# Kernel tuning notes

Hardware: AMD Instinct MI355X
Metric: run time of the kernel (lower is better)

## Reference

```python
import jax, jax.numpy as jnp
import numpy as np

# ---- Cl(3,0) geometric-algebra Cayley table (8 blades: 1,e1,e2,e3,e12,e13,e23,e123) ----
# T[k, i, j] = sign s.t. blade_i * blade_j = sign * blade_k (exactly 8 (i,j) pairs per k).

def _build_cayley():
    masks = [0b000, 0b001, 0b010, 0b100, 0b011, 0b101, 0b110, 0b111]
    T = np.zeros((8, 8, 8), np.float32)
    for i, a in enumerate(masks):
        for j, b in enumerate(masks):
            k = masks.index(a ^ b)
            aa, s = a >> 1, 0
            while aa:
                s += bin(aa & b).count('1')
                aa >>= 1
            T[k, i, j] = -1.0 if (s & 1) else 1.0
    return jnp.asarray(T)

CAYLEY = _build_cayley()
LN_EPS = 1e-5  # torch LayerNorm default


def _layer_norm(x, w, b):
    mu = jnp.mean(x, axis=-1, keepdims=True)
    var = jnp.var(x, axis=-1, keepdims=True)
    return (x - mu) * jax.lax.rsqrt(var + LN_EPS) * w + b


def _expert_forward(x_e, p_in, p_out, iw, gg, w_gate, w_up, w_down, lnw, lnb, out_w, out_b):
    # x_e: (C, D); p_in: (D, ED); per-round params indexed [r]
    C = x_e.shape[0]
    DB = lnw.shape[-1]
    mv = (x_e @ p_in).reshape(C, 8, DB)  # (C, n_blades, d_blade)
    n_rounds = iw.shape[0]
    for r in range(n_rounds):
        w = jax.nn.sigmoid(iw[r]).reshape(8, 8)          # interaction weights w[i,j]
        gate = jax.nn.sigmoid(gg[r])                      # scalar geo gate
        # geo[n,k,d] = sum_{i,j} sign[k,i,j] * w[i,j] * mv[n,i,d] * mv[n,j,d]
        geo = jnp.einsum('kij,ij,nid,njd->nkd', CAYLEY, w, mv, mv)
        mixed = gate * geo + (1.0 - gate) * mv
        flat = _layer_norm(mixed, lnw[r], lnb[r])         # LN over d_blade
        h = jax.nn.silu(flat @ w_gate[r]) * (flat @ w_up[r])  # SwiGLU
        mv = mv + h @ w_down[r]                           # residual
    out = mv.reshape(C, -1) @ p_out                       # (C, D)
    return _layer_norm(out, out_w, out_b)


def setup_inputs() -> dict:
    key = jax.random.key(0)
    ks = jax.random.split(key, 8)
    E, D, NB, DB, R, F = 16, 1024, 8, 64, 2, 256
    ED = NB * DB
    N = 32768
    C = N // E
    std = 0.02
    return {
        'x_sorted': jax.random.normal(ks[0], (N, D), jnp.float32),
        'proj_in': jax.random.normal(ks[1], (E, D, ED), jnp.float32) * std,
        'proj_out': jax.random.normal(ks[2], (E, ED, D), jnp.float32) * std,
        'interaction_weights': jnp.ones((E, R, 64), jnp.float32) * 0.1,
        'geo_gates': jnp.ones((E, R), jnp.float32) * 0.5,
        'ffn_gate': jax.random.normal(ks[3], (E, R, DB, F), jnp.float32) * std,
        'ffn_up': jax.random.normal(ks[4], (E, R, DB, F), jnp.float32) * std,
        'ffn_down': jax.random.normal(ks[5], (E, R, F, DB), jnp.float32) * std,
        'ffn_ln_w': jnp.ones((E, R, DB), jnp.float32),
        'ffn_ln_b': jnp.zeros((E, R, DB), jnp.float32),
        'out_ln_w': jnp.ones((D,), jnp.float32),
        'out_ln_b': jnp.zeros((D,), jnp.float32),
        'expert_offsets': jnp.arange(E, dtype=jnp.int32) * C,
        'expert_counts': jnp.full((E,), C, dtype=jnp.int32),
    }


def reference(x_sorted, proj_in, proj_out, interaction_weights, geo_gates,
              ffn_gate, ffn_up, ffn_down, ffn_ln_w, ffn_ln_b,
              out_ln_w, out_ln_b, expert_offsets, expert_counts):
    E = proj_in.shape[0]
    N, D = x_sorted.shape
    C = N // E  # balanced routing: equal tokens per expert (static shapes)
    idx = expert_offsets[:, None].astype(jnp.int32) + jnp.arange(C, dtype=jnp.int32)[None, :]
    x_b = x_sorted[idx]  # (E, C, D) gather of sorted tokens per expert
    y_b = jax.vmap(_expert_forward,
                   in_axes=(0, 0, 0, 0, 0, 0, 0, 0, 0, 0, None, None))(
        x_b, proj_in, proj_out, interaction_weights, geo_gates,
        ffn_gate, ffn_up, ffn_down, ffn_ln_w, ffn_ln_b, out_ln_w, out_ln_b)
    y = jnp.zeros_like(x_sorted).at[idx.reshape(-1)].set(y_b.reshape(-1, D))
    return y
```

## Files before the change

kernel.cpp:

```cpp
#include <hip/hip_runtime.h>

#define DEV __device__ __forceinline__

typedef __attribute__((ext_vector_type(4))) float f32x4;
typedef __attribute__((ext_vector_type(2))) float f32x2;
typedef __attribute__((ext_vector_type(8))) short bf16x8;


DEV unsigned short f2bf(float f) {
  union { float f; unsigned u; } v; v.f = f;
  unsigned r = v.u + 0x7fffu + ((v.u >> 16) & 1u);
  return (unsigned short)(r >> 16);
}

DEV unsigned pk2bf(float lo, float hi) {
  unsigned r;
  asm("v_cvt_pk_bf16_f32 %0, %1, %2" : "=v"(r) : "v"(lo), "v"(hi));
  return r;
}
DEV unsigned short f2bf1(float v) { return (unsigned short)pk2bf(v, v); }

DEV float bf2f(unsigned short b) {
  union { unsigned u; float f; } v; v.u = ((unsigned)b) << 16; return v.f;
}

DEV float frcp(float x) { return __builtin_amdgcn_rcpf(x); }

DEV void sbar() { asm volatile("s_barrier" ::: "memory"); }
DEV void wait_lgkm0() { asm volatile("s_waitcnt lgkmcnt(0)" ::: "memory"); }
DEV void wait_vm0() { asm volatile("s_waitcnt vmcnt(0)" ::: "memory"); }

DEV void async16(const unsigned short* g, unsigned short* l) {
  __builtin_amdgcn_global_load_lds(
      (__attribute__((address_space(1))) const unsigned int*)g,
      (__attribute__((address_space(3))) unsigned int*)l, 16, 0, 0);
}

DEV long tiled_off(long n, int k, int K) {
  return (n >> 3) * (8L * K) + (long)(((k >> 3) * 64) + ((int)(n & 7)) * 8 + (k & 7));
}

DEV bf16x8 ld_frag(const char* s, int row, int hi) {
  return *(const bf16x8*)(s + ((row >> 3) * 512 + hi * 128 + (row & 7) * 16));
}

__host__ __device__ constexpr int km_(int i) { return i==0?0:i==1?1:i==2?2:i==3?4:i==4?3:i==5?5:i==6?6:7; }
__host__ __device__ constexpr int pc_(int x) { int c = 0; while (x) { c += x & 1; x >>= 1; } return c; }
__host__ __device__ constexpr int KIDX(int i, int j) { return km_(km_(i) ^ km_(j)); }
__host__ __device__ constexpr int CSGN(int i, int j) {
  int a = km_(i), b = km_(j), aa = a >> 1, s = 0;
  while (aa) { s += pc_(aa & b); aa >>= 1; }
  return (s & 1) ? -1 : 1;
}
__host__ __device__ constexpr int PIDX(int i, int j) {
  return 8 * i - (i * (i - 1)) / 2 + (j - i);
}

__global__ __launch_bounds__(64) void geoprep_k(const float* __restrict__ iw,
                                                const float* __restrict__ gg,
                                                float* __restrict__ wcomb) {
  int er = threadIdx.x;
  if (er >= 32) return;
  const float* w = iw + er * 64;
  float gate = frcp(1.f + __expf(-gg[er]));
  float* c = wcomb + er * 40;
  int p = 0;
  for (int i = 0; i < 8; ++i)
    for (int j = i; j < 8; ++j) {
      float v = (float)CSGN(i, j) * frcp(1.f + __expf(-w[i * 8 + j]));
      if (j > i) v += (float)CSGN(j, i) * frcp(1.f + __expf(-w[j * 8 + i]));
      c[p++] = gate * v;
    }
  c[36] = 1.f - gate;
}

template<int TI>
__global__ __launch_bounds__(256) void transpose_k(const float* __restrict__ in,
                                                   unsigned short* __restrict__ out,
                                                   int Rr, int Cc) {
  __shared__ unsigned short tile[32][33];
  const float* ib = in + (long)blockIdx.z * Rr * Cc;
  unsigned short* ob = out + (long)blockIdx.z * Rr * Cc;
  int r0 = blockIdx.y * 32, c0 = blockIdx.x * 32;
  int tr = threadIdx.x >> 5, tc = threadIdx.x & 31;
#pragma unroll
  for (int i = 0; i < 4; ++i) {
    int r = tr + i * 8;
    tile[r][tc] = f2bf(ib[(long)(r0 + r) * Cc + c0 + tc]);
  }
  __syncthreads();
#pragma unroll
  for (int i = 0; i < 4; ++i) {
    int c = tr + i * 8;
    int row = c0 + c;
    int k = r0 + tc;
    if (TI == 0) ob[(long)row * Rr + k] = tile[tc][c];
    else ob[(long)row * Rr + (k ^ ((row & 7) << 3))] = tile[tc][c];
  }
}

__global__ __launch_bounds__(256) void trans_big_k(const float* __restrict__ in,
                                                   unsigned short* __restrict__ out,
                                                   int Rr, int Cc) {
  __shared__ float t[64][64];
  const float* ib = in + (long)blockIdx.z * Rr * Cc;
  unsigned short* ob = out + (long)blockIdx.z * (long)Rr * Cc;
  int k0 = blockIdx.y * 64, n0 = blockIdx.x * 64;
  int tid = threadIdx.x;
#pragma unroll
  for (int p = 0; p < 4; ++p) {
    int idx = p * 256 + tid;
    int kr = idx >> 4, nc = (idx & 15) * 4;
    *(float4*)&t[kr][nc] = *(const float4*)(ib + (long)(k0 + kr) * Cc + n0 + nc);
  }
  __syncthreads();
#pragma unroll
  for (int p = 0; p < 2; ++p) {
    int idx = p * 256 + tid;
    int n = idx & 63, kc = idx >> 6;
    float v[8];
#pragma unroll
    for (int u = 0; u < 8; ++u) v[u] = t[kc * 8 + u][n];
    uint4 o;
    o.x = pk2bf(v[0], v[1]); o.y = pk2bf(v[2], v[3]);
    o.z = pk2bf(v[4], v[5]); o.w = pk2bf(v[6], v[7]);
    *(uint4*)(ob + tiled_off(n0 + n, k0 + kc * 8, Rr)) = o;
  }
}

__global__ __launch_bounds__(512, 1) void gemm_in_k(const float* __restrict__ X,
                                                    const unsigned short* __restrict__ Bw,
                                                    unsigned short* __restrict__ MvB,
                                                    const int* __restrict__ offs) {
  extern __shared__ char smem[];
  int bid = blockIdx.x;
  int wg = (bid & 7) * 32 + (bid >> 3);
  int e = wg >> 4, rem = wg & 15, bm = rem >> 1, bn = rem & 1;
  int tid = threadIdx.x, wid = tid >> 6, lane = tid & 63;
  int wm = (wid >> 2) * 128, wn = (wid & 3) * 64;
  int ri = lane & 15, hi = lane >> 4;
  long rowbase = (long)offs[e] + bm * 256;
  long bw = (long)e * 64 + bn * 32;

  auto STGB = [&](int p) {
    int t = p >> 1, s = p & 1, b = t & 1;
    char* dst = smem + b * 65536 + 32768 + s * 16384;
#pragma unroll
    for (int i = 0; i < 2; ++i) {
      int d = i * 512 + tid;
      async16(Bw + (bw + (d >> 5)) * 8192 +
                  (long)((t * 8 + s * 4 + ((d >> 3) & 3)) * 64 + (d & 7) * 8),
              (unsigned short*)(dst + d * 16));
    }
  };
  auto A_LOAD = [&](int p, float4 ar[2][2]) {
    int t = p >> 1, s = p & 1;
#pragma unroll
    for (int i = 0; i < 2; ++i) {
      int d = i * 512 + tid;
      const float* src = X + (rowbase + ((d >> 5) * 8 + (d & 7))) * 1024 +
                         t * 64 + s * 32 + ((d >> 3) & 3) * 8;
      ar[i][0] = *(const float4*)src;
      ar[i][1] = *(const float4*)(src + 4);
    }
  };
  auto A_WRITE = [&](int p, float4 ar[2][2]) {
    int t = p >> 1, s = p & 1, b = t & 1;
    char* dst = smem + b * 65536 + s * 16384;
#pragma unroll
    for (int i = 0; i < 2; ++i) {
      int d = i * 512 + tid;
      uint4 o;
      o.x = pk2bf(ar[i][0].x, ar[i][0].y);
      o.y = pk2bf(ar[i][0].z, ar[i][0].w);
      o.z = pk2bf(ar[i][1].x, ar[i][1].y);
      o.w = pk2bf(ar[i][1].z, ar[i][1].w);
      *(uint4*)(dst + d * 16) = o;
    }
  };

  f32x4 acc[8][4];
#pragma unroll
  for (int i = 0; i < 8; ++i)
#pragma unroll
    for (int j = 0; j < 4; ++j) acc[i][j] = (f32x4){0.f, 0.f, 0.f, 0.f};

  float4 ar[2][2];
  A_LOAD(0, ar); STGB(0); STGB(1);
  A_WRITE(0, ar);
  A_LOAD(1, ar);
  A_WRITE(1, ar);
  wait_lgkm0();

#pragma unroll 2
  for (int p = 0; p < 32; ++p) {
    int t = p >> 1, s = p & 1, c = t & 1;
    if (p < 30) { A_LOAD(p + 2, ar); STGB(p + 2); }
    if (p < 30) asm volatile("s_waitcnt vmcnt(8)" ::: "memory");
    else if (p == 30) asm volatile("s_waitcnt vmcnt(2)" ::: "memory");
    else asm volatile("s_waitcnt vmcnt(0)" ::: "memory");
    sbar();
    const char* cA = smem + c * 65536 + s * 16384;
    const char* cB = smem + c * 65536 + 32768 + s * 16384;
    bf16x8 a[8], b[4];
#pragma unroll
    for (int i = 0; i < 8; ++i) a[i] = ld_frag(cA, wm + i * 16 + ri, hi);
#pragma unroll
    for (int j = 0; j < 4; ++j) b[j] = ld_frag(cB, wn + j * 16 + ri, hi);
    __builtin_amdgcn_s_setprio(1);
#pragma unroll
    for (int i = 0; i < 8; ++i)
#pragma unroll
      for (int j = 0; j < 4; ++j)
        acc[i][j] = __builtin_amdgcn_mfma_f32_16x16x32_bf16(a[i], b[j], acc[i][j], 0, 0, 0);
    __builtin_amdgcn_s_setprio(0);
    if (p < 30) A_WRITE(p + 2, ar);
    wait_lgkm0();
  }

  unsigned short* Cb = MvB + ((long)e * 2048 + (long)bm * 256) * 512 + bn * 256;
#pragma unroll
  for (int i = 0; i < 8; ++i)
#pragma unroll
    for (int j = 0; j < 4; ++j)
#pragma unroll
      for (int rr = 0; rr < 4; ++rr)
        Cb[(long)(wm + i * 16 + hi * 4 + rr) * 512 + wn + j * 16 + ri] =
            f2bf1(acc[i][j][rr]);
}

__global__ __launch_bounds__(256, 3) void rounds_k(
    const unsigned short* __restrict__ MvB, const unsigned short* __restrict__ WgT,
    const unsigned short* __restrict__ WuT, const unsigned short* __restrict__ WdT,
    const float* __restrict__ wcomb, const float* __restrict__ lnw,
    const float* __restrict__ lnb, unsigned short* __restrict__ Mvb) {
  extern __shared__ char smem[];
  int tid = threadIdx.x, wid = tid >> 6, lane = tid & 63;
  char* sFH = smem + wid * 4096;
  char* sMv = smem + 16384 + wid * 4096;
  char* sW  = smem + 32768;

  int bid = blockIdx.x;
  int wg = (bid & 7) * 256 + (bid >> 3);
  int e = wg >> 7, bx = wg & 127;

  int t4 = lane >> 4, q = lane & 15;
  int ri = lane & 15, hi = lane >> 4;
  int sw = (ri & 7) << 4;

  auto STAGE = [&](int i8) {
    long base = (long)(e * 2 + (i8 >> 3)) * 16384 + (i8 & 7) * 2048;
    char* dst = sW + (i8 & 1) * 8192;
    async16(WgT + base + tid * 8, (unsigned short*)(dst + tid * 16));
    async16(WuT + base + tid * 8, (unsigned short*)(dst + 4096 + tid * 16));
  };
  STAGE(0);

#pragma unroll 1
  for (int r = 0; r < 2; ++r) {
    int er = e * 2 + r;
    const unsigned short* wd = WdT + (long)er * 16384;

    f32x4 mv[8];
    if (r == 0) {
      long base = ((long)e * 2048 + bx * 16 + wid * 4 + t4) * 512 + 4 * q;
      uint2 uv[8];
#pragma unroll
      for (int i = 0; i < 8; ++i)
        uv[i] = *(const uint2*)(MvB + base + i * 64);
#pragma unroll
      for (int i = 0; i < 8; ++i) {
        *(uint2*)(sMv + t4 * 1024 + i * 128 + ((8 * q) ^ (i << 4))) = uv[i];
        mv[i] = (f32x4){bf2f((unsigned short)(uv[i].x & 0xffff)),
                        bf2f((unsigned short)(uv[i].x >> 16)),
                        bf2f((unsigned short)(uv[i].y & 0xffff)),
                        bf2f((unsigned short)(uv[i].y >> 16))};
      }
    } else {
#pragma unroll
      for (int i = 0; i < 8; ++i) {
        uint2 uv = *(const uint2*)(sMv + t4 * 1024 + i * 128 + ((8 * q) ^ (i << 4)));
        mv[i] = (f32x4){bf2f((unsigned short)(uv.x & 0xffff)),
                        bf2f((unsigned short)(uv.x >> 16)),
                        bf2f((unsigned short)(uv.y & 0xffff)),
                        bf2f((unsigned short)(uv.y >> 16))};
      }
    }

    {
      const float* C = wcomb + er * 40;
      f32x4 g[8];
#pragma unroll
      for (int k = 0; k < 8; ++k) g[k] = (f32x4){0.f, 0.f, 0.f, 0.f};
#pragma unroll
      for (int i = 0; i < 8; ++i)
#pragma unroll
        for (int j = i; j < 8; ++j) {
          float cc = C[PIDX(i, j)];
          const int k = KIDX(i, j);
          g[k] += cc * (mv[i] * mv[j]);
        }
      float omg = C[36];
#pragma unroll
      for (int k = 0; k < 8; ++k) g[k] = omg * mv[k] + g[k];
      float4 lw = *(const float4*)(lnw + (long)er * 64 + 4 * q);
      float4 lb = *(const float4*)(lnb + (long)er * 64 + 4 * q);
      f32x4 lwv = (f32x4){lw.x, lw.y, lw.z, lw.w};
      f32x4 lbv = (f32x4){lb.x, lb.y, lb.z, lb.w};
#pragma unroll
      for (int half = 0; half < 2; ++half) {
        f32x2 red[4];
#pragma unroll
        for (int k = 0; k < 4; ++k) {
          f32x4 m = g[half * 4 + k];
          red[k].x = (m.x + m.y) + (m.z + m.w);
          red[k].y = fmaf(m.x, m.x, m.y * m.y) + fmaf(m.z, m.z, m.w * m.w);
        }
#pragma unroll
        for (int off = 8; off >= 1; off >>= 1)
#pragma unroll
          for (int t = 0; t < 4; ++t) {
            f32x2 o;
            o.x = __shfl_xor(red[t].x, off);
            o.y = __shfl_xor(red[t].y, off);
            red[t] += o;
          }
#pragma unroll
        for (int k = 0; k < 4; ++k) {
          int kk = half * 4 + k;
          float mean = red[k].x * (1.f / 64.f);
          float var = red[k].y * (1.f / 64.f) - mean * mean;
          float rs = rsqrtf(var + 1e-5f);
          f32x4 nv = (g[kk] - mean) * rs;
          f32x4 ov = nv * lwv + lbv;
          uint2 pv;
          pv.x = pk2bf(ov.x, ov.y);
          pv.y = pk2bf(ov.z, ov.w);
          int row = t4 * 8 + kk;
          *(uint2*)(sFH + row * 128 + ((8 * q) ^ (kk << 4))) = pv;
        }
      }
    }
    wait_lgkm0();

    bf16x8 bfr[2][2];
#pragma unroll
    for (int tt = 0; tt < 2; ++tt)
#pragma unroll
      for (int kt = 0; kt < 2; ++kt)
        bfr[tt][kt] = *(const bf16x8*)(sFH + (tt * 16 + ri) * 128 + ((kt * 64 + hi * 16) ^ sw));

    f32x4 acc2[4][2];
#pragma unroll
    for (int j = 0; j < 4; ++j)
#pragma unroll
      for (int tt = 0; tt < 2; ++tt) acc2[j][tt] = (f32x4){0.f, 0.f, 0.f, 0.f};

#pragma unroll 1
    for (int q8 = 0; q8 < 8; ++q8) {
      int i8 = r * 8 + q8;
      wait_vm0();
      sbar();
      if (i8 < 15) STAGE(i8 + 1);

      bf16x8 wdf[4];
#pragma unroll
      for (int j = 0; j < 4; ++j)
        wdf[j] = *(const bf16x8*)(wd + (j * 16 + ri) * 256 + q8 * 32 + hi * 8);

      const char* bufW = sW + (i8 & 1) * 8192;

#pragma unroll
      for (int ftl = 0; ftl < 2; ++ftl) {
        const char* bg = bufW + (ftl * 16 + ri) * 128;
        const char* bu = bg + 4096;
        bf16x8 wg0 = *(const bf16x8*)(bg + ((hi * 16) ^ sw));
        bf16x8 wg1 = *(const bf16x8*)(bg + ((64 + hi * 16) ^ sw));
        bf16x8 wu0 = *(const bf16x8*)(bu + ((hi * 16) ^ sw));
        bf16x8 wu1 = *(const bf16x8*)(bu + ((64 + hi * 16) ^ sw));
        f32x4 ag[2], au[2];
#pragma unroll
        for (int tt = 0; tt < 2; ++tt) {
          ag[tt] = (f32x4){0.f, 0.f, 0.f, 0.f};
          au[tt] = (f32x4){0.f, 0.f, 0.f, 0.f};
        }
        __builtin_amdgcn_s_setprio(1);
#pragma unroll
        for (int tt = 0; tt < 2; ++tt) {
          ag[tt] = __builtin_amdgcn_mfma_f32_16x16x32_bf16(wg0, bfr[tt][0], ag[tt], 0, 0, 0);
          au[tt] = __builtin_amdgcn_mfma_f32_16x16x32_bf16(wu0, bfr[tt][0], au[tt], 0, 0, 0);
          ag[tt] = __builtin_amdgcn_mfma_f32_16x16x32_bf16(wg1, bfr[tt][1], ag[tt], 0, 0, 0);
          au[tt] = __builtin_amdgcn_mfma_f32_16x16x32_bf16(wu1, bfr[tt][1], au[tt], 0, 0, 0);
        }
        __builtin_amdgcn_s_setprio(0);
#pragma unroll
        for (int tt = 0; tt < 2; ++tt) {
          float hh[4];
#pragma unroll
          for (int rr = 0; rr < 4; ++rr) {
            float gv = ag[tt][rr], uu = au[tt][rr];
            hh[rr] = gv * uu * frcp(1.f + __expf(-gv));
          }
          uint2 hwv;
          hwv.x = pk2bf(hh[0], hh[1]);
          hwv.y = pk2bf(hh[2], hh[3]);
          *(uint2*)(sFH + (tt * 16 + ri) * 128 + ((ftl * 32 + hi * 8) ^ sw)) = hwv;
        }
      }
      wait_lgkm0();

      bf16x8 hk0 = *(const bf16x8*)(sFH + ri * 128 + ((hi * 16) ^ sw));
      bf16x8 hk1 = *(const bf16x8*)(sFH + (16 + ri) * 128 + ((hi * 16) ^ sw));
      __builtin_amdgcn_s_setprio(1);
#pragma unroll
      for (int j = 0; j < 4; ++j)
        acc2[j][0] = __builtin_amdgcn_mfma_f32_16x16x32_bf16(wdf[j], hk0, acc2[j][0], 0, 0, 0);
#pragma unroll
      for (int j = 0; j < 4; ++j)
        acc2[j][1] = __builtin_amdgcn_mfma_f32_16x16x32_bf16(wdf[j], hk1, acc2[j][1], 0, 0, 0);
      __builtin_amdgcn_s_setprio(0);
    }

    {
#pragma unroll
      for (int tt = 0; tt < 2; ++tt) {
        int tl = tt * 2 + (ri >> 3);
        int kb = ri & 7;
#pragma unroll
        for (int j = 0; j < 4; ++j)
#pragma unroll
          for (int u = 0; u < 2; ++u) {
            int off = (j * 32 + hi * 8 + 4 * u) ^ sw;
            unsigned* p = (unsigned*)(sMv + tl * 1024 + kb * 128 + off);
            unsigned old = *p;
            float v0 = bf2f((unsigned short)(old & 0xffff)) + acc2[j][tt][2 * u];
            float v1 = bf2f((unsigned short)(old >> 16)) + acc2[j][tt][2 * u + 1];
            *p = pk2bf(v0, v1);
          }
      }
    }
    wait_lgkm0();

    if (r == 1) {
      int tt = lane >> 4;
      int idx = lane & 15;
      int bl = idx >> 1;
      int c2 = idx & 1;
      const char* src = sMv + tt * 1024 + bl * 128;
      long row = (long)e * 2048 + bx * 16 + wid * 4 + tt;
      unsigned short* dst = Mvb + row * 512 + bl * 64 + c2 * 32;
#pragma unroll
      for (int h = 0; h < 4; ++h) {
        uint4 v = *(const uint4*)(src + ((c2 * 64 + h * 16) ^ (bl << 4)));
        *(uint4*)(dst + h * 8) = v;
      }
    }
  }
}

__global__ __launch_bounds__(512, 2) void gemm_out_ln_k(
    const unsigned short* __restrict__ Mvb, const unsigned short* __restrict__ Pw,
    float* __restrict__ Out, const float* __restrict__ ow, const float* __restrict__ ob,
    const int* __restrict__ offs) {
  extern __shared__ char smem[];
  int bid = blockIdx.x;
  int wg = (bid & 7) * 64 + (bid >> 3);
  int e = wg >> 5, mb = wg & 31;
  int tid = threadIdx.x, wid = tid >> 6, lane = tid & 63;
  int ri = lane & 15, hi = lane >> 4;
  long bbase = (long)e * 524288;
  long arow0 = (long)e * 2048 + (long)mb * 64;

  auto STAGE = [&](int buf, int kt) {
#pragma unroll
    for (int i = 0; i < 8; ++i) {
      int q = i * 512 + tid;
      int w = q >> 5, c = (q >> 3) & 3, rr = q & 7;
      async16(Pw + bbase + (long)w * 4096 + (kt * 4 + c) * 64 + rr * 8,
              (unsigned short*)(smem + buf * 65536 + q * 16));
    }
    if (tid < 256) {
      int q = tid;
      int w = q >> 5, c = (q >> 3) & 3, rr = q & 7;
      async16(Mvb + (arow0 + w * 8 + rr) * 512 + kt * 32 + c * 8,
              (unsigned short*)(smem + 131072 + buf * 4096 + q * 16));
    }
  };

  f32x4 acc[4][8];
#pragma unroll
  for (int i = 0; i < 4; ++i)
#pragma unroll
    for (int j = 0; j < 8; ++j) acc[i][j] = (f32x4){0.f, 0.f, 0.f, 0.f};

  STAGE(0, 0);
  for (int kt = 0; kt < 16; ++kt) {
    int cur = kt & 1;
    if (kt < 15) {
      STAGE(cur ^ 1, kt + 1);
      asm volatile("s_waitcnt vmcnt(8)" ::: "memory");
    } else {
      asm volatile("s_waitcnt vmcnt(0)" ::: "memory");
    }
    sbar();
    const char* cB = smem + cur * 65536;
    const char* cA = smem + 131072 + cur * 4096;
    bf16x8 a[4], b[8];
#pragma unroll
    for (int i = 0; i < 4; ++i) a[i] = ld_frag(cA, i * 16 + ri, hi);
#pragma unroll
    for (int j = 0; j < 8; ++j) b[j] = ld_frag(cB, wid * 128 + j * 16 + ri, hi);
    __builtin_amdgcn_s_setprio(1);
#pragma unroll
    for (int i = 0; i < 4; ++i)
#pragma unroll
      for (int j = 0; j < 8; ++j)
        acc[i][j] = __builtin_amdgcn_mfma_f32_16x16x32_bf16(a[i], b[j], acc[i][j], 0, 0, 0);
    __builtin_amdgcn_s_setprio(0);
    sbar();
  }

  float* rsum = (float*)(smem + 139264);
  float* rsq  = (float*)(smem + 141312);
  float* mexp = (float*)(smem + 143360);
  float* rstd = (float*)(smem + 143616);
  int hi4 = hi * 4;
#pragma unroll
  for (int i = 0; i < 4; ++i)
#pragma unroll
    for (int rr = 0; rr < 4; ++rr) {
      float s = 0.f, qv = 0.f;
#pragma unroll
      for (int j = 0; j < 8; ++j) { float v = acc[i][j][rr]; s += v; qv += v * v; }
#pragma unroll
      for (int off = 1; off < 16; off <<= 1) {
        s += __shfl_xor(s, off);
        qv += __shfl_xor(qv, off);
      }
      if (ri == 0) {
        int row = i * 16 + hi4 + rr;
        rsum[row * 8 + wid] = s;
        rsq[row * 8 + wid] = qv;
      }
    }
  __syncthreads();
  if (tid < 64) {
    float S = 0.f, Q = 0.f;
#pragma unroll
    for (int w = 0; w < 8; ++w) { S += rsum[tid * 8 + w]; Q += rsq[tid * 8 + w]; }
    float mean = S * (1.f / 1024.f);
    float var = Q * (1.f / 1024.f) - mean * mean;
    mexp[tid] = mean;
    rstd[tid] = rsqrtf(var + 1e-5f);
  }
  __syncthreads();
  long r0 = (long)offs[e] + (long)mb * 64;
  float owv[8], obv[8];
#pragma unroll
  for (int j = 0; j < 8; ++j) {
    int col = wid * 128 + j * 16 + ri;
    owv[j] = ow[col];
    obv[j] = ob[col];
  }
#pragma unroll
  for (int i = 0; i < 4; ++i)
#pragma unroll
    for (int rr = 0; rr < 4; ++rr) {
      int row = i * 16 + hi4 + rr;
      float mu = mexp[row], rs = rstd[row];
#pragma unroll
      for (int j = 0; j < 8; ++j) {
        int col = wid * 128 + j * 16 + ri;
        Out[(r0 + row) * 1024 + col] = (acc[i][j][rr] - mu) * rs * owv[j] + obv[j];
      }
    }
}

extern "C" void kernel_launch(void* const* d_in, const int* in_sizes, int n_in,
                              void* d_out, int out_size, void* d_ws, size_t ws_size,
                              hipStream_t stream) {
  const float* x    = (const float*)d_in[0];
  const float* pin  = (const float*)d_in[1];
  const float* pout = (const float*)d_in[2];
  const float* iw   = (const float*)d_in[3];
  const float* gg   = (const float*)d_in[4];
  const float* fg   = (const float*)d_in[5];
  const float* fu   = (const float*)d_in[6];
  const float* fd   = (const float*)d_in[7];
  const float* lnw  = (const float*)d_in[8];
  const float* lnb  = (const float*)d_in[9];
  const float* ow   = (const float*)d_in[10];
  const float* ob   = (const float*)d_in[11];
  const int* offs   = (const int*)d_in[12];

  char* ws = (char*)d_ws;
  unsigned short* mvB  = (unsigned short*)(ws + 0L);
  unsigned short* mvb  = (unsigned short*)(ws + 33554432L);
  unsigned short* pinT = (unsigned short*)(ws + 67108864L);
  unsigned short* poutT= (unsigned short*)(ws + 83886080L);
  unsigned short* wgT  = (unsigned short*)(ws + 100663296L);
  unsigned short* wuT  = (unsigned short*)(ws + 102760448L);
  unsigned short* wdT  = (unsigned short*)(ws + 104857600L);
  float* wcomb         = (float*)(ws + 106954752L);

  trans_big_k<<<dim3(8, 16, 16), dim3(256), 0, stream>>>(pin, pinT, 1024, 512);
  trans_big_k<<<dim3(16, 8, 16), dim3(256), 0, stream>>>(pout, poutT, 512, 1024);
  transpose_k<1><<<dim3(8, 2, 32), dim3(256), 0, stream>>>(fg, wgT, 64, 256);
  transpose_k<1><<<dim3(8, 2, 32), dim3(256), 0, stream>>>(fu, wuT, 64, 256);
  transpose_k<0><<<dim3(2, 8, 32), dim3(256), 0, stream>>>(fd, wdT, 256, 64);
  geoprep_k<<<dim3(1), dim3(64), 0, stream>>>(iw, gg, wcomb);

  gemm_in_k<<<dim3(256), dim3(512), 131072, stream>>>(x, pinT, mvB, offs);

  rounds_k<<<dim3(2048), dim3(256), 49152, stream>>>(
      mvB, wgT, wuT, wdT, wcomb, lnw, lnb, mvb);

  gemm_out_ln_k<<<dim3(512), dim3(512), 143872, stream>>>(
      mvb, poutT, (float*)d_out, ow, ob, offs);
}
```

Before: 274.4 us.

## Merge weight-prep kernels into one launch and keep rounds state in registers

Result: faster. 260.2 us (-5.2%).

```diff
diff --git a/kernel.cpp b/kernel.cpp
--- a/kernel.cpp
+++ b/kernel.cpp
@@ -22,6 +22,12 @@
 
 DEV float bf2f(unsigned short b) {
   union { unsigned u; float f; } v; v.u = ((unsigned)b) << 16; return v.f;
+}
+
+DEV unsigned addbf2(unsigned a, unsigned b) {
+  float lo = bf2f((unsigned short)(a & 0xffff)) + bf2f((unsigned short)(b & 0xffff));
+  float hi = bf2f((unsigned short)(a >> 16)) + bf2f((unsigned short)(b >> 16));
+  return pk2bf(lo, hi);
 }
 
 DEV float frcp(float x) { return __builtin_amdgcn_rcpf(x); }
@@ -56,11 +62,9 @@
   return 8 * i - (i * (i - 1)) / 2 + (j - i);
 }
 
-__global__ __launch_bounds__(64) void geoprep_k(const float* __restrict__ iw,
-                                                const float* __restrict__ gg,
-                                                float* __restrict__ wcomb) {
-  int er = threadIdx.x;
-  if (er >= 32) return;
+
+DEV void geoprep_body(const float* __restrict__ iw, const float* __restrict__ gg,
+                      float* __restrict__ wcomb, int er) {
   const float* w = iw + er * 64;
   float gate = frcp(1.f + __expf(-gg[er]));
   float* c = wcomb + er * 40;
@@ -75,14 +79,13 @@
 }
 
 template<int TI>
-__global__ __launch_bounds__(256) void transpose_k(const float* __restrict__ in,
-                                                   unsigned short* __restrict__ out,
-                                                   int Rr, int Cc) {
-  __shared__ unsigned short tile[32][33];
-  const float* ib = in + (long)blockIdx.z * Rr * Cc;
-  unsigned short* ob = out + (long)blockIdx.z * Rr * Cc;
-  int r0 = blockIdx.y * 32, c0 = blockIdx.x * 32;
-  int tr = threadIdx.x >> 5, tc = threadIdx.x & 31;
+DEV void transpose_body(const float* __restrict__ in, unsigned short* __restrict__ out,
+                        int Rr, int Cc, int bx, int by, int bz, int tid, char* sbuf) {
+  unsigned short (*tile)[33] = (unsigned short (*)[33])sbuf;
+  const float* ib = in + (long)bz * Rr * Cc;
+  unsigned short* ob = out + (long)bz * Rr * Cc;
+  int r0 = by * 32, c0 = bx * 32;
+  int tr = tid >> 5, tc = tid & 31;
 #pragma unroll
   for (int i = 0; i < 4; ++i) {
     int r = tr + i * 8;
@@ -99,14 +102,12 @@
   }
 }
 
-__global__ __launch_bounds__(256) void trans_big_k(const float* __restrict__ in,
-                                                   unsigned short* __restrict__ out,
-                                                   int Rr, int Cc) {
-  __shared__ float t[64][64];
-  const float* ib = in + (long)blockIdx.z * Rr * Cc;
-  unsigned short* ob = out + (long)blockIdx.z * (long)Rr * Cc;
-  int k0 = blockIdx.y * 64, n0 = blockIdx.x * 64;
-  int tid = threadIdx.x;
+DEV void trans_big_body(const float* __restrict__ in, unsigned short* __restrict__ out,
+                        int Rr, int Cc, int bx, int by, int bz, int tid, char* sbuf) {
+  float (*t)[64] = (float (*)[64])sbuf;
+  const float* ib = in + (long)bz * Rr * Cc;
+  unsigned short* ob = out + (long)bz * (long)Rr * Cc;
+  int k0 = by * 64, n0 = bx * 64;
 #pragma unroll
   for (int p = 0; p < 4; ++p) {
     int idx = p * 256 + tid;
@@ -125,6 +126,35 @@
     o.x = pk2bf(v[0], v[1]); o.y = pk2bf(v[2], v[3]);
     o.z = pk2bf(v[4], v[5]); o.w = pk2bf(v[6], v[7]);
     *(uint4*)(ob + tiled_off(n0 + n, k0 + kc * 8, Rr)) = o;
+  }
+}
+
+__global__ __launch_bounds__(256) void prep_k(
+    const float* __restrict__ pin, const float* __restrict__ pout,
+    const float* __restrict__ fg, const float* __restrict__ fu,
+    const float* __restrict__ fd, const float* __restrict__ iw,
+    const float* __restrict__ gg,
+    unsigned short* __restrict__ pinT, unsigned short* __restrict__ poutT,
+    unsigned short* __restrict__ wgT, unsigned short* __restrict__ wuT,
+    unsigned short* __restrict__ wdT, float* __restrict__ wcomb) {
+  __shared__ char sbuf[16384];
+  int b = blockIdx.x, tid = threadIdx.x;
+  if (b < 2048) {
+    trans_big_body(pin, pinT, 1024, 512, b & 7, (b >> 3) & 15, b >> 7, tid, sbuf);
+  } else if (b < 4096) {
+    int j = b - 2048;
+    trans_big_body(pout, poutT, 512, 1024, j & 15, (j >> 4) & 7, j >> 7, tid, sbuf);
+  } else if (b < 4608) {
+    int j = b - 4096;
+    transpose_body<1>(fg, wgT, 64, 256, j & 7, (j >> 3) & 1, j >> 4, tid, sbuf);
+  } else if (b < 5120) {
+    int j = b - 4608;
+    transpose_body<1>(fu, wuT, 64, 256, j & 7, (j >> 3) & 1, j >> 4, tid, sbuf);
+  } else if (b < 5632) {
+    int j = b - 5120;
+    transpose_body<0>(fd, wdT, 256, 64, j & 1, (j >> 1) & 7, j >> 4, tid, sbuf);
+  } else {
+    if (tid < 32) geoprep_body(iw, gg, wcomb, tid);
   }
 }
 
@@ -237,8 +267,7 @@
   extern __shared__ char smem[];
   int tid = threadIdx.x, wid = tid >> 6, lane = tid & 63;
   char* sFH = smem + wid * 4096;
-  char* sMv = smem + 16384 + wid * 4096;
-  char* sW  = smem + 32768;
+  char* sW  = smem + 16384;
 
   int bid = blockIdx.x;
   int wg = (bid & 7) * 256 + (bid >> 3);
@@ -256,36 +285,26 @@
   };
   STAGE(0);
 
+  uint2 uv[8];
+  {
+    long base = ((long)e * 2048 + bx * 16 + wid * 4 + t4) * 512 + 4 * q;
+#pragma unroll
+    for (int i = 0; i < 8; ++i)
+      uv[i] = *(const uint2*)(MvB + base + i * 64);
+  }
+
 #pragma unroll 1
   for (int r = 0; r < 2; ++r) {
     int er = e * 2 + r;
     const unsigned short* wd = WdT + (long)er * 16384;
 
     f32x4 mv[8];
-    if (r == 0) {
-      long base = ((long)e * 2048 + bx * 16 + wid * 4 + t4) * 512 + 4 * q;
-      uint2 uv[8];
-#pragma unroll
-      for (int i = 0; i < 8; ++i)
-        uv[i] = *(const uint2*)(MvB + base + i * 64);
-#pragma unroll
-      for (int i = 0; i < 8; ++i) {
-        *(uint2*)(sMv + t4 * 1024 + i * 128 + ((8 * q) ^ (i << 4))) = uv[i];
-        mv[i] = (f32x4){bf2f((unsigned short)(uv[i].x & 0xffff)),
-                        bf2f((unsigned short)(uv[i].x >> 16)),
-                        bf2f((unsigned short)(uv[i].y & 0xffff)),
-                        bf2f((unsigned short)(uv[i].y >> 16))};
-      }
-    } else {
-#pragma unroll
-      for (int i = 0; i < 8; ++i) {
-        uint2 uv = *(const uint2*)(sMv + t4 * 1024 + i * 128 + ((8 * q) ^ (i << 4)));
-        mv[i] = (f32x4){bf2f((unsigned short)(uv.x & 0xffff)),
-                        bf2f((unsigned short)(uv.x >> 16)),
-                        bf2f((unsigned short)(uv.y & 0xffff)),
-                        bf2f((unsigned short)(uv.y >> 16))};
-      }
-    }
+#pragma unroll
+    for (int i = 0; i < 8; ++i)
+      mv[i] = (f32x4){bf2f((unsigned short)(uv[i].x & 0xffff)),
+                      bf2f((unsigned short)(uv[i].x >> 16)),
+                      bf2f((unsigned short)(uv[i].y & 0xffff)),
+                      bf2f((unsigned short)(uv[i].y >> 16))};
 
     {
       const float* C = wcomb + er * 40;
@@ -427,33 +446,29 @@
         int tl = tt * 2 + (ri >> 3);
         int kb = ri & 7;
 #pragma unroll
-        for (int j = 0; j < 4; ++j)
-#pragma unroll
-          for (int u = 0; u < 2; ++u) {
-            int off = (j * 32 + hi * 8 + 4 * u) ^ sw;
-            unsigned* p = (unsigned*)(sMv + tl * 1024 + kb * 128 + off);
-            unsigned old = *p;
-            float v0 = bf2f((unsigned short)(old & 0xffff)) + acc2[j][tt][2 * u];
-            float v1 = bf2f((unsigned short)(old >> 16)) + acc2[j][tt][2 * u + 1];
-            *p = pk2bf(v0, v1);
-          }
+        for (int j = 0; j < 4; ++j) {
+          uint2 dv;
+          dv.x = pk2bf(acc2[j][tt][0], acc2[j][tt][1]);
+          dv.y = pk2bf(acc2[j][tt][2], acc2[j][tt][3]);
+          *(uint2*)(sFH + (tl * 8 + kb) * 128 + ((j * 32 + hi * 8) ^ (kb << 4))) = dv;
+        }
       }
+      wait_lgkm0();
+#pragma unroll
+      for (int i = 0; i < 8; ++i) {
+        uint2 dv = *(const uint2*)(sFH + (t4 * 8 + i) * 128 + ((8 * q) ^ (i << 4)));
+        uv[i].x = addbf2(uv[i].x, dv.x);
+        uv[i].y = addbf2(uv[i].y, dv.y);
+      }
     }
     wait_lgkm0();
 
     if (r == 1) {
-      int tt = lane >> 4;
-      int idx = lane & 15;
-      int bl = idx >> 1;
-      int c2 = idx & 1;
-      const char* src = sMv + tt * 1024 + bl * 128;
-      long row = (long)e * 2048 + bx * 16 + wid * 4 + tt;
-      unsigned short* dst = Mvb + row * 512 + bl * 64 + c2 * 32;
-#pragma unroll
-      for (int h = 0; h < 4; ++h) {
-        uint4 v = *(const uint4*)(src + ((c2 * 64 + h * 16) ^ (bl << 4)));
-        *(uint4*)(dst + h * 8) = v;
-      }
+      long row = (long)e * 2048 + bx * 16 + wid * 4 + t4;
+      unsigned short* dst = Mvb + row * 512 + 4 * q;
+#pragma unroll
+      for (int i = 0; i < 8; ++i)
+        *(uint2*)(dst + i * 64) = uv[i];
     }
   }
 }
@@ -603,16 +618,12 @@
   unsigned short* wdT  = (unsigned short*)(ws + 104857600L);
   float* wcomb         = (float*)(ws + 106954752L);
 
-  trans_big_k<<<dim3(8, 16, 16), dim3(256), 0, stream>>>(pin, pinT, 1024, 512);
-  trans_big_k<<<dim3(16, 8, 16), dim3(256), 0, stream>>>(pout, poutT, 512, 1024);
-  transpose_k<1><<<dim3(8, 2, 32), dim3(256), 0, stream>>>(fg, wgT, 64, 256);
-  transpose_k<1><<<dim3(8, 2, 32), dim3(256), 0, stream>>>(fu, wuT, 64, 256);
-  transpose_k<0><<<dim3(2, 8, 32), dim3(256), 0, stream>>>(fd, wdT, 256, 64);
-  geoprep_k<<<dim3(1), dim3(64), 0, stream>>>(iw, gg, wcomb);
+  prep_k<<<dim3(5633), dim3(256), 0, stream>>>(
+      pin, pout, fg, fu, fd, iw, gg, pinT, poutT, wgT, wuT, wdT, wcomb);
 
   gemm_in_k<<<dim3(256), dim3(512), 131072, stream>>>(x, pinT, mvB, offs);
 
-  rounds_k<<<dim3(2048), dim3(256), 49152, stream>>>(
+  rounds_k<<<dim3(2048), dim3(256), 32768, stream>>>(
       mvB, wgT, wuT, wdT, wcomb, lnw, lnb, mvb);
 
   gemm_out_ln_k<<<dim3(512), dim3(512), 143872, stream>>>(
```
